# Optimization experiments

Hardware: AMD Instinct MI355X
Metric: run time of the kernel (lower is better)

## Reference

```python
import jax, jax.numpy as jnp
import numpy as np

# Detector / Siddon constants (from init_kwargs)
H, W = 200, 200
DELX, DELY = 1.5, 1.5
NXV, NYV, NZV = 256, 256, 256  # voxel counts
EPS = 1e-8


def setup_inputs() -> dict:
    key = jax.random.key(0)
    kvol, = jax.random.split(key, 1)
    volume = jax.random.uniform(kvol, (NXV, NYV, NZV), dtype=jnp.float32)  # CT intensities
    spacing = jnp.ones((3,), jnp.float32)                                  # 1mm isotropic
    sdr = jnp.array([300.0], jnp.float32)                                  # source-to-detector radius
    rotations = jnp.array([[0.5, -0.2, 0.3]], jnp.float32)                 # theta, phi, gamma
    translations = jnp.array([[128.0, 128.0, 128.0]], jnp.float32)         # volume center (bx,by,bz)
    return {"volume": volume, "spacing": spacing, "sdr": sdr,
            "rotations": rotations, "translations": translations}


def _rotation_matrix(rotations):
    # R = Rz(theta) @ Ry(phi) @ Rx(gamma), batched
    theta, phi, gamma = rotations[:, 0], rotations[:, 1], rotations[:, 2]
    ct, st = jnp.cos(theta), jnp.sin(theta)
    cp, sp = jnp.cos(phi), jnp.sin(phi)
    cg, sg = jnp.cos(gamma), jnp.sin(gamma)
    z = jnp.zeros_like(theta)
    o = jnp.ones_like(theta)
    Rz = jnp.stack([ct, -st, z, st, ct, z, z, z, o], -1).reshape(-1, 3, 3)
    Ry = jnp.stack([cp, z, sp, z, o, z, -sp, z, cp], -1).reshape(-1, 3, 3)
    Rx = jnp.stack([o, z, z, z, cg, -sg, z, sg, cg], -1).reshape(-1, 3, 3)
    return Rz @ Ry @ Rx


def _make_xrays(sdr, rotations, translations):
    # Detector.make_xrays: source on column 0 of sdr*R, detector center opposite,
    # detector plane spanned by unit columns 1 and 2.
    R = _rotation_matrix(rotations)                 # (b,3,3), orthonormal columns
    source = sdr[:, None] * R[..., 0]               # (b,3)
    center = -source
    basis = jnp.stack([R[..., 1], R[..., 2]], 1)    # (b,2,3)
    source = source + translations
    center = center + translations
    t = (jnp.arange(-(H // 2), H // 2, dtype=jnp.float32) + 1.0) * DELX
    s = (jnp.arange(-(W // 2), W // 2, dtype=jnp.float32) + 1.0) * DELY
    coefs = jnp.stack(jnp.meshgrid(t, s, indexing="ij"), -1).reshape(-1, 2)  # (H*W,2) == cartesian_prod(t,s)
    target = jnp.einsum("bcd,nc->bnd", basis, coefs) + center[:, None, :]    # (b,n,3)
    return source[:, None, :], target               # (b,1,3), (b,n,3)


def reference(volume, spacing, sdr, rotations, translations):
    source, target = _make_xrays(sdr, rotations, translations)
    vol = jnp.flip(volume, 0)                       # Siddon flips axis 0
    nx, ny, nz = vol.shape
    sdd = target - source + EPS                     # (b,n,3) ray directions

    # Alphas at every axis-aligned plane intersection: P = (nx+1)+(ny+1)+(nz+1)
    alphas = jnp.concatenate(
        [(jnp.arange(n + 1, dtype=jnp.float32) * spacing[i] - source[..., i:i + 1]) / sdd[..., i:i + 1]
         for i, n in enumerate((nx, ny, nz))], axis=-1)          # (b,n,P)

    # Entry/exit alphas of the volume bounding box
    extent = jnp.asarray([nx, ny, nz], jnp.float32) * spacing
    a0 = (0.0 - source) / sdd
    a1 = (extent - source) / sdd
    amin = jnp.max(jnp.minimum(a0, a1), -1, keepdims=True)       # (b,n,1)
    amax = jnp.min(jnp.maximum(a0, a1), -1, keepdims=True)

    # Out-of-range alphas -> sentinel amax (sorts to the end, contributes zero step;
    # equivalent to the original's NaN + nansum handling)
    valid = (alphas >= amin) & (alphas <= amax)
    alphas = jnp.sort(jnp.where(valid, alphas, amax), axis=-1)

    mid = 0.5 * (alphas[..., :-1] + alphas[..., 1:])             # (b,n,P-1)
    step = jnp.diff(alphas, axis=-1)

    # Midpoint positions -> voxel indices (trunc, clamped in-bounds)
    xyz = source[:, :, None, :] + mid[..., None] * sdd[:, :, None, :]  # (b,n,P-1,3)
    idx = jnp.trunc(xyz / spacing).astype(jnp.int32)
    ix = jnp.clip(idx[..., 0], 0, nx - 1)
    iy = jnp.clip(idx[..., 1], 0, ny - 1)
    iz = jnp.clip(idx[..., 2], 0, nz - 1)
    voxels = vol[ix, iy, iz]                                     # gather, (b,n,P-1)

    drr = jnp.sum(voxels * step, -1) * jnp.linalg.norm(sdd, axis=-1)
    return drr.reshape(-1, H, W)
```

## Files before the change

### kernel.cpp

```cpp
#include <hip/hip_runtime.h>

#define H_ 200
#define W_ 200
#define DELX_ 1.5f
#define DELY_ 1.5f
#define NXV_ 256
#define NYV_ 256
#define NZV_ 256
#define EPS_ 1e-8f
#define NSEG 8
#define PPB 32

__device__ __forceinline__ float alpha_mul(float k, float sp, float src, float inv_sdd) {
    return (k * sp - src) * inv_sdd;
}

__global__ void __launch_bounds__(256)
drr_fused(const float* __restrict__ vol,
          const float* __restrict__ spacing,
          const float* __restrict__ sdr,
          const float* __restrict__ rot,
          const float* __restrict__ trans,
          float* __restrict__ out,
          int B) {
    const int npix = B * H_ * W_;
    const int t = threadIdx.x;
    const int pixLocal = t & (PPB - 1);
    const int seg = t >> 5;
    const int pix = blockIdx.x * PPB + pixLocal;
    const bool active = pix < npix;

    float result = 0.0f;
    if (active) {
        const int b = pix / (H_ * W_);
        const int p = pix % (H_ * W_);
        const int i = p / W_, j = p % W_;

        const float theta = rot[b * 3 + 0], phi = rot[b * 3 + 1], gamma = rot[b * 3 + 2];
        const float ct = cosf(theta), st = sinf(theta);
        const float cp = cosf(phi),   sp = sinf(phi);
        const float cg = cosf(gamma), sg = sinf(gamma);
        const float r00 = ct * cp,                r10 = st * cp,                r20 = -sp;
        const float r01 = ct * sp * sg - st * cg, r11 = st * sp * sg + ct * cg, r21 = cp * sg;
        const float r02 = ct * sp * cg + st * sg, r12 = st * sp * cg - ct * sg, r22 = cp * cg;

        const float sd = sdr[b];
        const float tx = trans[b * 3 + 0], ty = trans[b * 3 + 1], tz = trans[b * 3 + 2];
        const float sx = sd * r00 + tx, sy = sd * r10 + ty, sz = sd * r20 + tz;
        const float cxx = -sd * r00 + tx, cyy = -sd * r10 + ty, czz = -sd * r20 + tz;

        const float tco = ((float)(i - H_ / 2) + 1.0f) * DELX_;
        const float sco = ((float)(j - W_ / 2) + 1.0f) * DELY_;
        const float gx = r01 * tco + r02 * sco + cxx;
        const float gy = r11 * tco + r12 * sco + cyy;
        const float gz = r21 * tco + r22 * sco + czz;

        const float dx = gx - sx + EPS_;
        const float dy = gy - sy + EPS_;
        const float dz = gz - sz + EPS_;

        const float spx = spacing[0], spy = spacing[1], spz = spacing[2];
        const float inv_spx = 1.0f / spx, inv_spy = 1.0f / spy, inv_spz = 1.0f / spz;
        const float inv_dx = 1.0f / dx, inv_dy = 1.0f / dy, inv_dz = 1.0f / dz;

        const float a0x = alpha_mul(0.f, spx, sx, inv_dx), a1x = alpha_mul((float)NXV_, spx, sx, inv_dx);
        const float a0y = alpha_mul(0.f, spy, sy, inv_dy), a1y = alpha_mul((float)NYV_, spy, sy, inv_dy);
        const float a0z = alpha_mul(0.f, spz, sz, inv_dz), a1z = alpha_mul((float)NZV_, spz, sz, inv_dz);

        const float amin = fmaxf(fmaxf(fminf(a0x, a1x), fminf(a0y, a1y)), fminf(a0z, a1z));
        const float amax = fminf(fminf(fmaxf(a0x, a1x), fmaxf(a0y, a1y)), fmaxf(a0z, a1z));

        const float norm = sqrtf(dx * dx + dy * dy + dz * dz);

        const float klo = (float)(seg * (NXV_ / NSEG));
        const float khi = (float)((seg + 1) * (NXV_ / NSEG));
        const float aA = alpha_mul(klo, spx, sx, inv_dx);
        const float aB = alpha_mul(khi, spx, sx, inv_dx);
        const float lo = fminf(aA, aB), hi = fmaxf(aA, aB);

        const float start = fmaxf(amin, lo);
        const float end   = fminf(amax, hi);

        float acc = 0.0f;
        if (start < end) {
            float kx, ky, kz, axv, ayv, azv, dkx, dky, dkz;
            {
                float kf = (start * dx + sx) * inv_spx;
                if (dx > 0.f) { dkx = 1.f;  kx = floorf(kf) + 1.f; }
                else          { dkx = -1.f; kx = ceilf(kf) - 1.f; }
                axv = alpha_mul(kx, spx, sx, inv_dx);
            }
            {
                float kf = (start * dy + sy) * inv_spy;
                if (dy > 0.f) { dky = 1.f;  ky = floorf(kf) + 1.f; }
                else          { dky = -1.f; ky = ceilf(kf) - 1.f; }
                ayv = alpha_mul(ky, spy, sy, inv_dy);
            }
            {
                float kf = (start * dz + sz) * inv_spz;
                if (dz > 0.f) { dkz = 1.f;  kz = floorf(kf) + 1.f; }
                else          { dkz = -1.f; kz = ceilf(kf) - 1.f; }
                azv = alpha_mul(kz, spz, sz, inv_dz);
            }

            float a_cur = start;
            int it = 0;
            while (it++ < 512) {
                float an = fminf(axv, fminf(ayv, azv));
                if (an > end) break;
                float stp = an - a_cur;
                float midv = 0.5f * (a_cur + an);
                float x = (sx + midv * dx) * inv_spx;
                float y = (sy + midv * dy) * inv_spy;
                float z = (sz + midv * dz) * inv_spz;
                int ix = (int)x;
                int iy = (int)y;
                int iz = (int)z;
                ix = min(max(ix, 0), NXV_ - 1);
                iy = min(max(iy, 0), NYV_ - 1);
                iz = min(max(iz, 0), NZV_ - 1);
                float v = vol[((NXV_ - 1 - ix) * NYV_ + iy) * NZV_ + iz];
                acc += v * stp;
                a_cur = an;
                if (axv == an) { kx += dkx; axv = alpha_mul(kx, spx, sx, inv_dx); }
                if (ayv == an) { ky += dky; ayv = alpha_mul(ky, spy, sy, inv_dy); }
                if (azv == an) { kz += dkz; azv = alpha_mul(kz, spz, sz, inv_dz); }
            }
        }
        result = acc * norm;
    }

    __shared__ float red[NSEG * PPB];
    red[t] = result;
    __syncthreads();
    if (t < PPB && active) {
        float s = 0.0f;
        #pragma unroll
        for (int k = 0; k < NSEG; k++) s += red[t + k * PPB];
        out[pix] = s;
    }
}

extern "C" void kernel_launch(void* const* d_in, const int* in_sizes, int n_in,
                              void* d_out, int out_size, void* d_ws, size_t ws_size,
                              hipStream_t stream) {
    const float* vol     = (const float*)d_in[0];
    const float* spacing = (const float*)d_in[1];
    const float* sdr     = (const float*)d_in[2];
    const float* rot     = (const float*)d_in[3];
    const float* trans   = (const float*)d_in[4];
    float* out = (float*)d_out;

    const int B = in_sizes[2];
    const int npix = B * H_ * W_;
    const int nblocks = (npix + PPB - 1) / PPB;
    drr_fused<<<nblocks, NSEG * PPB, 0, stream>>>(vol, spacing, sdr, rot, trans, out, B);
}
```

Baseline: 145.6 us.

## Use 2D pixel tiles and unroll Siddon traversal to batch voxel gathers

New measurement: 126.1 us. 13.4% less time.

```diff
diff --git a/kernel.cpp b/kernel.cpp
--- a/kernel.cpp
+++ b/kernel.cpp
@@ -10,6 +10,9 @@
 #define EPS_ 1e-8f
 #define NSEG 8
 #define PPB 32
+#define TILE_R 8
+#define TILE_C 4
+#define TILES_PER_IMG ((H_ / TILE_R) * (W_ / TILE_C))
 
 __device__ __forceinline__ float alpha_mul(float k, float sp, float src, float inv_sdd) {
     return (k * sp - src) * inv_sdd;
@@ -21,94 +24,96 @@
           const float* __restrict__ sdr,
           const float* __restrict__ rot,
           const float* __restrict__ trans,
-          float* __restrict__ out,
-          int B) {
-    const int npix = B * H_ * W_;
+          float* __restrict__ out) {
     const int t = threadIdx.x;
     const int pixLocal = t & (PPB - 1);
     const int seg = t >> 5;
-    const int pix = blockIdx.x * PPB + pixLocal;
-    const bool active = pix < npix;
 
-    float result = 0.0f;
-    if (active) {
-        const int b = pix / (H_ * W_);
-        const int p = pix % (H_ * W_);
-        const int i = p / W_, j = p % W_;
+    const int b   = blockIdx.x / TILES_PER_IMG;
+    const int rem = blockIdx.x % TILES_PER_IMG;
+    const int ty  = rem / (W_ / TILE_C);
+    const int tx  = rem % (W_ / TILE_C);
+    const int i = ty * TILE_R + (pixLocal >> 2);
+    const int j = tx * TILE_C + (pixLocal & 3);
+    const int pix = b * (H_ * W_) + i * W_ + j;
 
-        const float theta = rot[b * 3 + 0], phi = rot[b * 3 + 1], gamma = rot[b * 3 + 2];
-        const float ct = cosf(theta), st = sinf(theta);
-        const float cp = cosf(phi),   sp = sinf(phi);
-        const float cg = cosf(gamma), sg = sinf(gamma);
-        const float r00 = ct * cp,                r10 = st * cp,                r20 = -sp;
-        const float r01 = ct * sp * sg - st * cg, r11 = st * sp * sg + ct * cg, r21 = cp * sg;
-        const float r02 = ct * sp * cg + st * sg, r12 = st * sp * cg - ct * sg, r22 = cp * cg;
+    const float theta = rot[b * 3 + 0], phi = rot[b * 3 + 1], gamma = rot[b * 3 + 2];
+    const float ct = cosf(theta), st = sinf(theta);
+    const float cp = cosf(phi),   sp = sinf(phi);
+    const float cg = cosf(gamma), sg = sinf(gamma);
+    const float r00 = ct * cp,                r10 = st * cp,                r20 = -sp;
+    const float r01 = ct * sp * sg - st * cg, r11 = st * sp * sg + ct * cg, r21 = cp * sg;
+    const float r02 = ct * sp * cg + st * sg, r12 = st * sp * cg - ct * sg, r22 = cp * cg;
 
-        const float sd = sdr[b];
-        const float tx = trans[b * 3 + 0], ty = trans[b * 3 + 1], tz = trans[b * 3 + 2];
-        const float sx = sd * r00 + tx, sy = sd * r10 + ty, sz = sd * r20 + tz;
-        const float cxx = -sd * r00 + tx, cyy = -sd * r10 + ty, czz = -sd * r20 + tz;
+    const float sd = sdr[b];
+    const float tx_ = trans[b * 3 + 0], ty_ = trans[b * 3 + 1], tz_ = trans[b * 3 + 2];
+    const float sx = sd * r00 + tx_, sy = sd * r10 + ty_, sz = sd * r20 + tz_;
+    const float cxx = -sd * r00 + tx_, cyy = -sd * r10 + ty_, czz = -sd * r20 + tz_;
 
-        const float tco = ((float)(i - H_ / 2) + 1.0f) * DELX_;
-        const float sco = ((float)(j - W_ / 2) + 1.0f) * DELY_;
-        const float gx = r01 * tco + r02 * sco + cxx;
-        const float gy = r11 * tco + r12 * sco + cyy;
-        const float gz = r21 * tco + r22 * sco + czz;
+    const float tco = ((float)(i - H_ / 2) + 1.0f) * DELX_;
+    const float sco = ((float)(j - W_ / 2) + 1.0f) * DELY_;
+    const float gx = r01 * tco + r02 * sco + cxx;
+    const float gy = r11 * tco + r12 * sco + cyy;
+    const float gz = r21 * tco + r22 * sco + czz;
 
-        const float dx = gx - sx + EPS_;
-        const float dy = gy - sy + EPS_;
-        const float dz = gz - sz + EPS_;
+    const float dx = gx - sx + EPS_;
+    const float dy = gy - sy + EPS_;
+    const float dz = gz - sz + EPS_;
 
-        const float spx = spacing[0], spy = spacing[1], spz = spacing[2];
-        const float inv_spx = 1.0f / spx, inv_spy = 1.0f / spy, inv_spz = 1.0f / spz;
-        const float inv_dx = 1.0f / dx, inv_dy = 1.0f / dy, inv_dz = 1.0f / dz;
+    const float spx = spacing[0], spy = spacing[1], spz = spacing[2];
+    const float inv_spx = 1.0f / spx, inv_spy = 1.0f / spy, inv_spz = 1.0f / spz;
+    const float inv_dx = 1.0f / dx, inv_dy = 1.0f / dy, inv_dz = 1.0f / dz;
 
-        const float a0x = alpha_mul(0.f, spx, sx, inv_dx), a1x = alpha_mul((float)NXV_, spx, sx, inv_dx);
-        const float a0y = alpha_mul(0.f, spy, sy, inv_dy), a1y = alpha_mul((float)NYV_, spy, sy, inv_dy);
-        const float a0z = alpha_mul(0.f, spz, sz, inv_dz), a1z = alpha_mul((float)NZV_, spz, sz, inv_dz);
+    const float a0x = alpha_mul(0.f, spx, sx, inv_dx), a1x = alpha_mul((float)NXV_, spx, sx, inv_dx);
+    const float a0y = alpha_mul(0.f, spy, sy, inv_dy), a1y = alpha_mul((float)NYV_, spy, sy, inv_dy);
+    const float a0z = alpha_mul(0.f, spz, sz, inv_dz), a1z = alpha_mul((float)NZV_, spz, sz, inv_dz);
 
-        const float amin = fmaxf(fmaxf(fminf(a0x, a1x), fminf(a0y, a1y)), fminf(a0z, a1z));
-        const float amax = fminf(fminf(fmaxf(a0x, a1x), fmaxf(a0y, a1y)), fmaxf(a0z, a1z));
+    const float amin = fmaxf(fmaxf(fminf(a0x, a1x), fminf(a0y, a1y)), fminf(a0z, a1z));
+    const float amax = fminf(fminf(fmaxf(a0x, a1x), fmaxf(a0y, a1y)), fmaxf(a0z, a1z));
 
-        const float norm = sqrtf(dx * dx + dy * dy + dz * dz);
+    const float norm = sqrtf(dx * dx + dy * dy + dz * dz);
 
-        const float klo = (float)(seg * (NXV_ / NSEG));
-        const float khi = (float)((seg + 1) * (NXV_ / NSEG));
-        const float aA = alpha_mul(klo, spx, sx, inv_dx);
-        const float aB = alpha_mul(khi, spx, sx, inv_dx);
-        const float lo = fminf(aA, aB), hi = fmaxf(aA, aB);
+    const float klo = (float)(seg * (NXV_ / NSEG));
+    const float khi = (float)((seg + 1) * (NXV_ / NSEG));
+    const float aA = alpha_mul(klo, spx, sx, inv_dx);
+    const float aB = alpha_mul(khi, spx, sx, inv_dx);
+    const float lo = fminf(aA, aB), hi = fmaxf(aA, aB);
 
-        const float start = fmaxf(amin, lo);
-        const float end   = fminf(amax, hi);
+    const float start = fmaxf(amin, lo);
+    const float end   = fminf(amax, hi);
 
-        float acc = 0.0f;
-        if (start < end) {
-            float kx, ky, kz, axv, ayv, azv, dkx, dky, dkz;
-            {
-                float kf = (start * dx + sx) * inv_spx;
-                if (dx > 0.f) { dkx = 1.f;  kx = floorf(kf) + 1.f; }
-                else          { dkx = -1.f; kx = ceilf(kf) - 1.f; }
-                axv = alpha_mul(kx, spx, sx, inv_dx);
-            }
-            {
-                float kf = (start * dy + sy) * inv_spy;
-                if (dy > 0.f) { dky = 1.f;  ky = floorf(kf) + 1.f; }
-                else          { dky = -1.f; ky = ceilf(kf) - 1.f; }
-                ayv = alpha_mul(ky, spy, sy, inv_dy);
-            }
-            {
-                float kf = (start * dz + sz) * inv_spz;
-                if (dz > 0.f) { dkz = 1.f;  kz = floorf(kf) + 1.f; }
-                else          { dkz = -1.f; kz = ceilf(kf) - 1.f; }
-                azv = alpha_mul(kz, spz, sz, inv_dz);
-            }
+    float acc = 0.0f;
+    if (start < end) {
+        float kx, ky, kz, axv, ayv, azv, dkx, dky, dkz;
+        {
+            float kf = (start * dx + sx) * inv_spx;
+            if (dx > 0.f) { dkx = 1.f;  kx = floorf(kf) + 1.f; }
+            else          { dkx = -1.f; kx = ceilf(kf) - 1.f; }
+            axv = alpha_mul(kx, spx, sx, inv_dx);
+        }
+        {
+            float kf = (start * dy + sy) * inv_spy;
+            if (dy > 0.f) { dky = 1.f;  ky = floorf(kf) + 1.f; }
+            else          { dky = -1.f; ky = ceilf(kf) - 1.f; }
+            ayv = alpha_mul(ky, spy, sy, inv_dy);
+        }
+        {
+            float kf = (start * dz + sz) * inv_spz;
+            if (dz > 0.f) { dkz = 1.f;  kz = floorf(kf) + 1.f; }
+            else          { dkz = -1.f; kz = ceilf(kf) - 1.f; }
+            azv = alpha_mul(kz, spz, sz, inv_dz);
+        }
 
-            float a_cur = start;
-            int it = 0;
-            while (it++ < 512) {
+        float a_cur = start;
+        for (int g = 0; g < 40; ++g) {
+            float stp[4];
+            int   off[4];
+            float an_last;
+            #pragma unroll
+            for (int u = 0; u < 4; ++u) {
                 float an = fminf(axv, fminf(ayv, azv));
-                if (an > end) break;
-                float stp = an - a_cur;
+                bool ok = (an <= end);
+                stp[u] = ok ? (an - a_cur) : 0.0f;
                 float midv = 0.5f * (a_cur + an);
                 float x = (sx + midv * dx) * inv_spx;
                 float y = (sy + midv * dy) * inv_spy;
@@ -119,25 +124,41 @@
                 ix = min(max(ix, 0), NXV_ - 1);
                 iy = min(max(iy, 0), NYV_ - 1);
                 iz = min(max(iz, 0), NZV_ - 1);
-                float v = vol[((NXV_ - 1 - ix) * NYV_ + iy) * NZV_ + iz];
-                acc += v * stp;
+                off[u] = ((NXV_ - 1 - ix) * NYV_ + iy) * NZV_ + iz;
                 a_cur = an;
-                if (axv == an) { kx += dkx; axv = alpha_mul(kx, spx, sx, inv_dx); }
-                if (ayv == an) { ky += dky; ayv = alpha_mul(ky, spy, sy, inv_dy); }
-                if (azv == an) { kz += dkz; azv = alpha_mul(kz, spz, sz, inv_dz); }
+                bool cx = (axv == an), cy = (ayv == an), cz = (azv == an);
+                kx = cx ? kx + dkx : kx;
+                ky = cy ? ky + dky : ky;
+                kz = cz ? kz + dkz : kz;
+                axv = alpha_mul(kx, spx, sx, inv_dx);
+                ayv = alpha_mul(ky, spy, sy, inv_dy);
+                azv = alpha_mul(kz, spz, sz, inv_dz);
+                an_last = an;
             }
+            float v0 = vol[off[0]];
+            float v1 = vol[off[1]];
+            float v2 = vol[off[2]];
+            float v3 = vol[off[3]];
+            acc += v0 * stp[0];
+            acc += v1 * stp[1];
+            acc += v2 * stp[2];
+            acc += v3 * stp[3];
+            if (an_last > end) break;
         }
-        result = acc * norm;
     }
+    float result = acc * norm;
 
     __shared__ float red[NSEG * PPB];
     red[t] = result;
     __syncthreads();
-    if (t < PPB && active) {
+    if (t < PPB) {
+        const int ii = ty * TILE_R + (t >> 2);
+        const int jj = tx * TILE_C + (t & 3);
+        const int opix = b * (H_ * W_) + ii * W_ + jj;
         float s = 0.0f;
         #pragma unroll
         for (int k = 0; k < NSEG; k++) s += red[t + k * PPB];
-        out[pix] = s;
+        out[opix] = s;
     }
 }
 
@@ -152,7 +173,6 @@
     float* out = (float*)d_out;
 
     const int B = in_sizes[2];
-    const int npix = B * H_ * W_;
-    const int nblocks = (npix + PPB - 1) / PPB;
-    drr_fused<<<nblocks, NSEG * PPB, 0, stream>>>(vol, spacing, sdr, rot, trans, out, B);
+    const int nblocks = B * TILES_PER_IMG;
+    drr_fused<<<nblocks, NSEG * PPB, 0, stream>>>(vol, spacing, sdr, rot, trans, out);
 }
```
